# Kernel tuning notes

Measured on AMD Instinct MI355X. Metric: run time of the kernel, lower is better.

## Reference

```python
import jax, jax.numpy as jnp
import numpy as np

HIDDEN = 2048
HEADS = 16
HEAD_DIM = HIDDEN // HEADS          # 128
HALF = HEAD_DIM // 2                # 64
LATENT = HIDDEN // 4                # 512 (compression_ratio=4)
ROPE_BASE = 10000.0


def _rope_cos_sin(seq_len):
    # LlamaRotaryEmbedding with dim=HALF
    inv_freq = 1.0 / (ROPE_BASE ** (jnp.arange(0, HALF, 2, dtype=jnp.float32) / HALF))
    t = jnp.arange(seq_len, dtype=jnp.float32)
    freqs = jnp.einsum('i,j->ij', t, inv_freq)          # [S, HALF/2]
    emb = jnp.concatenate([freqs, freqs], axis=-1)       # [S, HALF]
    cos = jnp.cos(emb)[None, :, None, :]                 # [1,S,1,HALF]
    sin = jnp.sin(emb)[None, :, None, :]
    return cos, sin


def _rotate_half(x):
    x1, x2 = jnp.split(x, 2, axis=-1)
    return jnp.concatenate([-x2, x1], axis=-1)


def _apply_rope(x, cos, sin):
    return x * cos + _rotate_half(x) * sin


def setup_inputs() -> dict:
    key = jax.random.key(0)
    ks = jax.random.split(key, 10)
    B, S = 2, 2048
    std = 0.02
    inp = {
        'x':        jax.random.normal(ks[0], (B, S, HIDDEN), jnp.float32),
        # weights stored as [in, out] (transposed torch Linear weight)
        'W_kv_d':   jax.random.normal(ks[1], (HIDDEN, LATENT), jnp.float32) * std,
        'W_q_d':    jax.random.normal(ks[2], (HIDDEN, LATENT), jnp.float32) * std,
        'W_k_u':    jax.random.normal(ks[3], (LATENT, HEADS * HALF), jnp.float32) * std,
        'W_q_u':    jax.random.normal(ks[4], (LATENT, HEADS * HALF), jnp.float32) * std,
        'W_v_u':    jax.random.normal(ks[5], (LATENT, HIDDEN), jnp.float32) * std,
        'W_rope_k': jax.random.normal(ks[6], (HIDDEN, HIDDEN // 2), jnp.float32) * std,
        'W_rope_q': jax.random.normal(ks[7], (LATENT, HIDDEN // 2), jnp.float32) * std,
        'W_o':      jax.random.normal(ks[8], (HIDDEN, HIDDEN), jnp.float32) * std,
    }
    return inp


def reference(x, W_kv_d, W_q_d, W_k_u, W_q_u, W_v_u, W_rope_k, W_rope_q, W_o):
    B, S, _ = x.shape
    kv_latent = x @ W_kv_d                      # [B,S,LATENT]
    q_latent = x @ W_q_d                        # [B,S,LATENT]

    k = (kv_latent @ W_k_u).reshape(B, S, HEADS, HALF)
    q = (q_latent @ W_q_u).reshape(B, S, HEADS, HALF)
    v = (kv_latent @ W_v_u).reshape(B, S, HEADS, HEAD_DIM)

    q_rope = (q_latent @ W_rope_q).reshape(B, S, HEADS, HALF)
    k_rope = (x @ W_rope_k).reshape(B, S, HEADS, HALF)

    cos, sin = _rope_cos_sin(S)
    k_rope = _apply_rope(k_rope, cos, sin)
    q_rope = _apply_rope(q_rope, cos, sin)

    q = jnp.concatenate([q, q_rope], axis=-1)   # [B,S,H,HEAD_DIM]
    k = jnp.concatenate([k, k_rope], axis=-1)

    scale = 1.0 / jnp.sqrt(jnp.float32(HEAD_DIM))
    scores = jnp.einsum('bqhd,bkhd->bhqk', q, k) * scale   # [B,H,S,S]
    causal = jnp.tril(jnp.ones((S, S), dtype=bool))
    scores = jnp.where(causal[None, None], scores, jnp.float32(-1e30))
    attn = jax.nn.softmax(scores, axis=-1)
    y = jnp.einsum('bhqk,bkhd->bqhd', attn, v).reshape(B, S, HIDDEN)
    return y @ W_o
```

## Files before the change

kernel.cpp:

```cpp
#include <hip/hip_runtime.h>
#include <hip/hip_bf16.h>

typedef __hip_bfloat16 bf16;
typedef __attribute__((ext_vector_type(8))) short short8;
typedef __attribute__((ext_vector_type(4))) float f32x4;

#define AS1 __attribute__((address_space(1)))
#define AS3 __attribute__((address_space(3)))

__device__ __forceinline__ void gload_lds16(const bf16* gp, bf16* lp) {
  __builtin_amdgcn_global_load_lds((const AS1 void*)gp, (AS3 void*)lp, 16, 0, 0);
}

__device__ __forceinline__ float fast_exp2(float x) {
#if __has_builtin(__builtin_amdgcn_exp2f)
  return __builtin_amdgcn_exp2f(x);
#else
  return exp2f(x);
#endif
}

__device__ __forceinline__ void store_c(bf16* C, size_t idx, float v) { C[idx] = __float2bfloat16(v); }
__device__ __forceinline__ void store_c(float* C, size_t idx, float v) { C[idx] = v; }

struct __align__(8) b16x4 { bf16 a, b, c, d; };

__global__ void cvt_f32_bf16(const float* __restrict__ in, bf16* __restrict__ out) {
  const int i = (blockIdx.x * 256 + threadIdx.x) * 4;
  const float4 v = *(const float4*)(in + i);
  out[i + 0] = __float2bfloat16(v.x);
  out[i + 1] = __float2bfloat16(v.y);
  out[i + 2] = __float2bfloat16(v.z);
  out[i + 3] = __float2bfloat16(v.w);
}

__global__ void rope_tab_kernel(float2* __restrict__ ctab) {
  const int idx = blockIdx.x * 256 + threadIdx.x;
  const int i = idx & 31;
  const int s = idx >> 5;
  const float inv = fast_exp2(-(float)i * 0.41524101186092029f);
  const float ang = (float)s * inv;
  ctab[idx] = make_float2(cosf(ang), sinf(ang));
}

struct PrepArgs {
  const float* src[8];
  bf16* dst[8];
  int R[8], C[8], cum[8];
};

__global__ void prep_kernel(PrepArgs a) {
  __shared__ bf16 t[32][33];
  const int blk = blockIdx.x;
  int e = 0;
  while (e < 7 && blk >= a.cum[e]) ++e;
  const int lt = blk - (e ? a.cum[e - 1] : 0);
  const int R = a.R[e], C = a.C[e];
  const int tpr = C >> 5;
  const int bx = lt % tpr, by = lt / tpr;
  const float* in = a.src[e];
  bf16* out = a.dst[e];
  const int c0 = bx * 32, r0 = by * 32;
  const int tx = threadIdx.x, ty = threadIdx.y;
  for (int i = 0; i < 4; ++i)
    t[ty + 8 * i][tx] = __float2bfloat16(in[(size_t)(r0 + ty + 8 * i) * C + c0 + tx]);
  __syncthreads();
  for (int i = 0; i < 4; ++i)
    out[(size_t)(c0 + ty + 8 * i) * R + r0 + tx] = t[tx][ty + 8 * i];
}

template <typename CT, int MODE>
__global__ void gemm_bt(const bf16* __restrict__ A, int lda,
                        const bf16* __restrict__ Bt,
                        CT* __restrict__ C, bf16* __restrict__ C2, int ldc,
                        int K, const float2* __restrict__ ctab)
{
  __shared__ __align__(16) bf16 As[2][128 * 32];
  __shared__ __align__(16) bf16 Bs[2][128 * 32];
  const int tid  = threadIdx.x;
  const int wave = tid >> 6, lane = tid & 63;
  const int quad = lane >> 4, l16 = lane & 15;
  const int m0 = blockIdx.y * 128, n0 = blockIdx.x * 128;
  const int wm = (wave >> 1) * 64, wn = (wave & 1) * 64;

  f32x4 acc[4][4];
#pragma unroll
  for (int i = 0; i < 4; ++i)
#pragma unroll
    for (int j = 0; j < 4; ++j) acc[i][j] = (f32x4){0.f, 0.f, 0.f, 0.f};

  const int r1  = tid >> 2;
  const int ks1 = (tid & 3) * 8;

  gload_lds16(A  + (size_t)(m0 + r1)      * lda + ks1, &As[0][tid * 8]);
  gload_lds16(A  + (size_t)(m0 + r1 + 64) * lda + ks1, &As[0][(tid + 256) * 8]);
  gload_lds16(Bt + (size_t)(n0 + r1)      * K   + ks1, &Bs[0][tid * 8]);
  gload_lds16(Bt + (size_t)(n0 + r1 + 64) * K   + ks1, &Bs[0][(tid + 256) * 8]);

  int cur = 0;
  for (int k0 = 0; k0 < K; k0 += 32) {
    if (k0 + 32 < K) {
      const int kn = k0 + 32;
      const int nxt = cur ^ 1;
      gload_lds16(A  + (size_t)(m0 + r1)      * lda + kn + ks1, &As[nxt][tid * 8]);
      gload_lds16(A  + (size_t)(m0 + r1 + 64) * lda + kn + ks1, &As[nxt][(tid + 256) * 8]);
      gload_lds16(Bt + (size_t)(n0 + r1)      * K   + kn + ks1, &Bs[nxt][tid * 8]);
      gload_lds16(Bt + (size_t)(n0 + r1 + 64) * K   + kn + ks1, &Bs[nxt][(tid + 256) * 8]);
      asm volatile("s_waitcnt vmcnt(4)" ::: "memory");
    } else {
      asm volatile("s_waitcnt vmcnt(0)" ::: "memory");
    }
    __builtin_amdgcn_s_barrier();

    short8 af[4], bf_[4];
#pragma unroll
    for (int mt = 0; mt < 4; ++mt)
      af[mt] = *(const short8*)&As[cur][(wm + mt * 16 + l16) * 32 + quad * 8];
#pragma unroll
    for (int nt = 0; nt < 4; ++nt)
      bf_[nt] = *(const short8*)&Bs[cur][(wn + nt * 16 + l16) * 32 + quad * 8];
#pragma unroll
    for (int mt = 0; mt < 4; ++mt)
#pragma unroll
      for (int nt = 0; nt < 4; ++nt)
        acc[mt][nt] = __builtin_amdgcn_mfma_f32_16x16x32_bf16(af[mt], bf_[nt], acc[mt][nt], 0, 0, 0);
    __builtin_amdgcn_s_barrier();
    cur ^= 1;
  }

  if (MODE == 0) {
#pragma unroll
    for (int mt = 0; mt < 4; ++mt) {
      const int row = m0 + wm + mt * 16 + quad * 4;
#pragma unroll
      for (int nt = 0; nt < 4; ++nt) {
        const int cn = n0 + wn + nt * 16 + l16;
        const f32x4 v = acc[mt][nt];
#pragma unroll
        for (int r = 0; r < 4; ++r)
          store_c(C, (size_t)(row + r) * ldc + cn, v[r]);
      }
    }
  } else if (MODE == 4) {
    if (n0 < 1024) {
#pragma unroll
      for (int mt = 0; mt < 4; ++mt) {
        const int row = m0 + wm + mt * 16 + quad * 4;
#pragma unroll
        for (int nt = 0; nt < 4; ++nt) {
          const int cn = n0 + wn + nt * 16 + l16;
          const f32x4 v = acc[mt][nt];
#pragma unroll
          for (int r = 0; r < 4; ++r)
            store_c(C, (size_t)(row + r) * 1024 + cn, v[r]);
        }
      }
    } else {
#pragma unroll
      for (int mt = 0; mt < 4; ++mt) {
        const int row = m0 + wm + mt * 16 + quad * 4;
        f32x4 w[4];
#pragma unroll
        for (int nt = 0; nt < 4; ++nt) w[nt] = acc[mt][nt];
#pragma unroll
        for (int r = 0; r < 4; ++r) {
          const int s = (row + r) & 2047;
          const float2 cs0 = ctab[(s << 5) + l16];
          const float2 cs1 = ctab[(s << 5) + 16 + l16];
          const float x1a = w[0][r], x2a = w[2][r];
          const float x1b = w[1][r], x2b = w[3][r];
          w[0][r] = x1a * cs0.x - x2a * cs0.y;
          w[2][r] = x2a * cs0.x + x1a * cs0.y;
          w[1][r] = x1b * cs1.x - x2b * cs1.y;
          w[3][r] = x2b * cs1.x + x1b * cs1.y;
        }
#pragma unroll
        for (int nt = 0; nt < 4; ++nt) {
          const int cn2 = n0 + wn + nt * 16 + l16 - 1024;
          const int g = ((cn2 >> 6) << 7) + 64 + (cn2 & 63);
#pragma unroll
          for (int r = 0; r < 4; ++r)
            C2[(size_t)(row + r) * 2048 + g] = __float2bfloat16(w[nt][r]);
        }
      }
    }
  }
}

__global__ void gemm_up_fused(const bf16* __restrict__ latcat,
                              const bf16* __restrict__ wtUP,
                              const bf16* __restrict__ wtQcat,
                              bf16* __restrict__ vT, bf16* __restrict__ kfull,
                              bf16* __restrict__ qfull,
                              const float2* __restrict__ ctab)
{
  const bool is2 = (blockIdx.x >= 24);
  const bf16* A  = latcat + (is2 ? 512 : 0);
  const bf16* Bt = is2 ? wtQcat : wtUP;
  const int n0 = (is2 ? (int)blockIdx.x - 24 : (int)blockIdx.x) * 128;
  const int K = 512, lda = 1024;

  __shared__ __align__(16) bf16 As[2][128 * 32];
  __shared__ __align__(16) bf16 Bs[2][128 * 32];
  const int tid  = threadIdx.x;
  const int wave = tid >> 6, lane = tid & 63;
  const int quad = lane >> 4, l16 = lane & 15;
  const int m0 = blockIdx.y * 128;
  const int wm = (wave >> 1) * 64, wn = (wave & 1) * 64;

  f32x4 acc[4][4];
#pragma unroll
  for (int i = 0; i < 4; ++i)
#pragma unroll
    for (int j = 0; j < 4; ++j) acc[i][j] = (f32x4){0.f, 0.f, 0.f, 0.f};

  const int r1  = tid >> 2;
  const int ks1 = (tid & 3) * 8;

  gload_lds16(A  + (size_t)(m0 + r1)      * lda + ks1, &As[0][tid * 8]);
  gload_lds16(A  + (size_t)(m0 + r1 + 64) * lda + ks1, &As[0][(tid + 256) * 8]);
  gload_lds16(Bt + (size_t)(n0 + r1)      * K   + ks1, &Bs[0][tid * 8]);
  gload_lds16(Bt + (size_t)(n0 + r1 + 64) * K   + ks1, &Bs[0][(tid + 256) * 8]);

  int cur = 0;
  for (int k0 = 0; k0 < K; k0 += 32) {
    if (k0 + 32 < K) {
      const int kn = k0 + 32;
      const int nxt = cur ^ 1;
      gload_lds16(A  + (size_t)(m0 + r1)      * lda + kn + ks1, &As[nxt][tid * 8]);
      gload_lds16(A  + (size_t)(m0 + r1 + 64) * lda + kn + ks1, &As[nxt][(tid + 256) * 8]);
      gload_lds16(Bt + (size_t)(n0 + r1)      * K   + kn + ks1, &Bs[nxt][tid * 8]);
      gload_lds16(Bt + (size_t)(n0 + r1 + 64) * K   + kn + ks1, &Bs[nxt][(tid + 256) * 8]);
      asm volatile("s_waitcnt vmcnt(4)" ::: "memory");
    } else {
      asm volatile("s_waitcnt vmcnt(0)" ::: "memory");
    }
    __builtin_amdgcn_s_barrier();

    short8 af[4], bf_[4];
#pragma unroll
    for (int mt = 0; mt < 4; ++mt)
      af[mt] = *(const short8*)&As[cur][(wm + mt * 16 + l16) * 32 + quad * 8];
#pragma unroll
    for (int nt = 0; nt < 4; ++nt)
      bf_[nt] = *(const short8*)&Bs[cur][(wn + nt * 16 + l16) * 32 + quad * 8];
#pragma unroll
    for (int mt = 0; mt < 4; ++mt)
#pragma unroll
      for (int nt = 0; nt < 4; ++nt)
        acc[mt][nt] = __builtin_amdgcn_mfma_f32_16x16x32_bf16(af[mt], bf_[nt], acc[mt][nt], 0, 0, 0);
    __builtin_amdgcn_s_barrier();
    cur ^= 1;
  }

  if (is2) {
    if (n0 < 1024) {
#pragma unroll
      for (int mt = 0; mt < 4; ++mt) {
        const int row = m0 + wm + mt * 16 + quad * 4;
#pragma unroll
        for (int nt = 0; nt < 4; ++nt) {
          const int cn = n0 + wn + nt * 16 + l16;
          const int g = (((cn >> 6) & 15) << 7) + ((cn >> 10) << 6) + (cn & 63);
          const f32x4 v = acc[mt][nt];
#pragma unroll
          for (int r = 0; r < 4; ++r)
            qfull[(size_t)(row + r) * 2048 + g] = __float2bfloat16(v[r]);
        }
      }
    } else {
#pragma unroll
      for (int mt = 0; mt < 4; ++mt) {
        const int row = m0 + wm + mt * 16 + quad * 4;
        f32x4 w[4];
#pragma unroll
        for (int nt = 0; nt < 4; ++nt) w[nt] = acc[mt][nt];
#pragma unroll
        for (int r = 0; r < 4; ++r) {
          const int s = (row + r) & 2047;
          const float2 cs0 = ctab[(s << 5) + l16];
          const float2 cs1 = ctab[(s << 5) + 16 + l16];
          const float x1a = w[0][r], x2a = w[2][r];
          const float x1b = w[1][r], x2b = w[3][r];
          w[0][r] = x1a * cs0.x - x2a * cs0.y;
          w[2][r] = x2a * cs0.x + x1a * cs0.y;
          w[1][r] = x1b * cs1.x - x2b * cs1.y;
          w[3][r] = x2b * cs1.x + x1b * cs1.y;
        }
#pragma unroll
        for (int nt = 0; nt < 4; ++nt) {
          const int cn = n0 + wn + nt * 16 + l16;
          const int g = (((cn >> 6) & 15) << 7) + ((cn >> 10) << 6) + (cn & 63);
#pragma unroll
          for (int r = 0; r < 4; ++r)
            qfull[(size_t)(row + r) * 2048 + g] = __float2bfloat16(w[nt][r]);
        }
      }
    }
  } else {
#pragma unroll
    for (int mt = 0; mt < 4; ++mt) {
      const int row = m0 + wm + mt * 16 + quad * 4;
#pragma unroll
      for (int nt = 0; nt < 4; ++nt) {
        const int cn = n0 + wn + nt * 16 + l16;
        const f32x4 v = acc[mt][nt];
        if (cn < 1024) {
          const int g = ((cn >> 6) << 7) + (cn & 63);
#pragma unroll
          for (int r = 0; r < 4; ++r)
            kfull[(size_t)(row + r) * 2048 + g] = __float2bfloat16(v[r]);
        } else {
          const int cn2 = cn - 1024;
          const int bb = row >> 11, s0 = row & 2047;
          b16x4 pk;
          pk.a = __float2bfloat16(v[0]); pk.b = __float2bfloat16(v[1]);
          pk.c = __float2bfloat16(v[2]); pk.d = __float2bfloat16(v[3]);
          *(b16x4*)(vT + ((size_t)(bb * 2048 + cn2)) * 2048 + s0) = pk;
        }
      }
    }
  }
}

__device__ __forceinline__ void attn_phase(
    const bf16* __restrict__ Q, const bf16* __restrict__ Kf,
    const bf16* __restrict__ VT,
    size_t kqbase, size_t vtbase, int qt, int t0, int t1,
    bf16* __restrict__ Ks, bf16* __restrict__ VTs, bf16* __restrict__ Psw,
    f32x4 (&o)[2][8], f32x4 (&lacc)[2], const short8 ones,
    int wave, int quad, int l16, int krow, int kcol, int vrow, int vcol)
{
  const float C2 = 0.08838834764831845f * 1.4426950408889634f;
  const float MNEG = -30.0f;
  const int wq0 = qt * 128 + wave * 32;

  short8 qf[2][4];
#pragma unroll
  for (int m = 0; m < 2; ++m) {
    const bf16* qp = Q + kqbase + (size_t)(wq0 + m * 16 + l16) * 2048 + quad * 8;
#pragma unroll
    for (int kc = 0; kc < 4; ++kc) qf[m][kc] = *(const short8*)(qp + kc * 32);
  }

  short8 kg[4], vg[4];
  {
    const int kk = t0 * 64;
#pragma unroll
    for (int i = 0; i < 4; ++i)
      kg[i] = *(const short8*)(Kf + kqbase + (size_t)(kk + krow + i * 16) * 2048 + kcol);
#pragma unroll
    for (int i = 0; i < 4; ++i)
      vg[i] = *(const short8*)(VT + vtbase + (size_t)(vrow + i * 32) * 2048 + kk + vcol);
  }

  for (int t = t0; t < t1; ++t) {
    const int k0 = t * 64;
    __syncthreads();
#pragma unroll
    for (int i = 0; i < 4; ++i) {
      const int rw = krow + i * 16;
      *(short8*)&Ks[rw * 128 + (kcol ^ ((rw & 7) * 8))] = kg[i];
    }
#pragma unroll
    for (int i = 0; i < 4; ++i) {
      const int rw = vrow + i * 32;
      *(short8*)&VTs[rw * 64 + (vcol ^ ((rw & 7) * 8))] = vg[i];
    }
    __syncthreads();
    if (t + 1 < t1) {
      const int kn = k0 + 64;
#pragma unroll
      for (int i = 0; i < 4; ++i)
        kg[i] = *(const short8*)(Kf + kqbase + (size_t)(kn + krow + i * 16) * 2048 + kcol);
#pragma unroll
      for (int i = 0; i < 4; ++i)
        vg[i] = *(const short8*)(VT + vtbase + (size_t)(vrow + i * 32) * 2048 + kn + vcol);
    }
    if (k0 > wq0 + 31) continue;

    f32x4 sf[2][4];
#pragma unroll
    for (int kt = 0; kt < 4; ++kt) {
      sf[0][kt] = (f32x4){0, 0, 0, 0};
      sf[1][kt] = (f32x4){0, 0, 0, 0};
    }
#pragma unroll
    for (int kt = 0; kt < 4; ++kt) {
#pragma unroll
      for (int kc = 0; kc < 4; ++kc) {
        const short8 bfr = *(const short8*)&Ks[(kt * 16 + l16) * 128 +
                                              ((kc * 32 + quad * 8) ^ ((l16 & 7) * 8))];
        sf[0][kt] = __builtin_amdgcn_mfma_f32_16x16x32_bf16(qf[0][kc], bfr, sf[0][kt], 0, 0, 0);
        sf[1][kt] = __builtin_amdgcn_mfma_f32_16x16x32_bf16(qf[1][kc], bfr, sf[1][kt], 0, 0, 0);
      }
    }
#pragma unroll
    for (int m = 0; m < 2; ++m) {
      const int row0m = wq0 + m * 16 + quad * 4;
      if (k0 + 63 > row0m) {
#pragma unroll
        for (int kt = 0; kt < 4; ++kt) {
          const int col = k0 + kt * 16 + l16;
#pragma unroll
          for (int r = 0; r < 4; ++r)
            sf[m][kt][r] = (col > row0m + r) ? -3e38f : sf[m][kt][r];
        }
      }
    }
#pragma unroll
    for (int m = 0; m < 2; ++m)
#pragma unroll
      for (int kt = 0; kt < 4; ++kt)
#pragma unroll
        for (int r = 0; r < 4; ++r) {
          const float p = fast_exp2(__builtin_fmaf(sf[m][kt][r], C2, MNEG));
          const int prow = m * 16 + quad * 4 + r;
          const int pcol = (kt * 16 + l16) ^ (quad * 16);
          Psw[prow * 64 + pcol] = __float2bfloat16(p);
        }
    asm volatile("s_waitcnt lgkmcnt(0)" ::: "memory");
#pragma unroll
    for (int kc = 0; kc < 2; ++kc) {
      short8 ap[2];
      const int acol = (kc * 32 + quad * 8) ^ (((l16 >> 2) & 3) * 16);
      ap[0] = *(const short8*)&Psw[l16 * 64 + acol];
      lacc[0] = __builtin_amdgcn_mfma_f32_16x16x32_bf16(ap[0], ones, lacc[0], 0, 0, 0);
      ap[1] = *(const short8*)&Psw[(16 + l16) * 64 + acol];
      lacc[1] = __builtin_amdgcn_mfma_f32_16x16x32_bf16(ap[1], ones, lacc[1], 0, 0, 0);
#pragma unroll
      for (int dt = 0; dt < 8; ++dt) {
        const short8 vb = *(const short8*)&VTs[(dt * 16 + l16) * 64 +
                                              ((kc * 32 + quad * 8) ^ ((l16 & 7) * 8))];
        o[0][dt] = __builtin_amdgcn_mfma_f32_16x16x32_bf16(ap[0], vb, o[0][dt], 0, 0, 0);
        o[1][dt] = __builtin_amdgcn_mfma_f32_16x16x32_bf16(ap[1], vb, o[1][dt], 0, 0, 0);
      }
    }
  }
}

__global__ __launch_bounds__(256, 2) void attn10_kernel(
    const bf16* __restrict__ Q, const bf16* __restrict__ Kf,
    const bf16* __restrict__ VT, bf16* __restrict__ Y,
    bf16* __restrict__ poA, float* __restrict__ lA, float* __restrict__ lB)
{
  __shared__ __align__(16) bf16 Ks[64 * 128];
  __shared__ __align__(16) bf16 VTs[128 * 64];
  __shared__ __align__(16) bf16 Ps[4 * 32 * 64];
  const int tid  = threadIdx.x;
  const int wave = tid >> 6, lane = tid & 63;
  const int quad = lane >> 4, l16 = lane & 15;
  const int bh = blockIdx.x;
  const int j  = blockIdx.y;
  const int qt_A = 15 - j;
  const int qt_B = j;
  const size_t kqbase = ((size_t)(bh >> 4) * 2048) * 2048 + (bh & 15) * 128;
  const size_t vtbase = (size_t)bh * 128 * 2048;

  short8 ones;
#pragma unroll
  for (int i = 0; i < 8; ++i) ones[i] = (short)0x3F80;

  const int krow = tid >> 4, kcol = (tid & 15) * 8;
  const int vrow = tid >> 3, vcol = (tid & 7) * 8;
  bf16* Psw = Ps + wave * (32 * 64);

  f32x4 o[2][8];
  f32x4 lacc[2];

#pragma unroll
  for (int m = 0; m < 2; ++m)
#pragma unroll
    for (int i = 0; i < 8; ++i) o[m][i] = (f32x4){0, 0, 0, 0};
  lacc[0] = (f32x4){0, 0, 0, 0};
  lacc[1] = (f32x4){0, 0, 0, 0};
  attn_phase(Q, Kf, VT, kqbase, vtbase, qt_A, qt_A + 1, 2 * qt_A + 2,
             Ks, VTs, Psw, o, lacc, ones, wave, quad, l16, krow, kcol, vrow, vcol);
  {
    bf16* po = poA + ((size_t)(bh * 16 + qt_A) << 14);
    float* pl = lA + ((bh * 16 + qt_A) << 7);
#pragma unroll
    for (int m = 0; m < 2; ++m)
#pragma unroll
      for (int r = 0; r < 4; ++r) {
        const int rl = wave * 32 + m * 16 + quad * 4 + r;
#pragma unroll
        for (int dt = 0; dt < 8; ++dt)
          po[rl * 128 + dt * 16 + l16] = __float2bfloat16(o[m][dt][r]);
        if (l16 == 0) pl[rl] = lacc[m][r];
      }
  }

#pragma unroll
  for (int m = 0; m < 2; ++m)
#pragma unroll
    for (int i = 0; i < 8; ++i) o[m][i] = (f32x4){0, 0, 0, 0};
  lacc[0] = (f32x4){0, 0, 0, 0};
  lacc[1] = (f32x4){0, 0, 0, 0};
  attn_phase(Q, Kf, VT, kqbase, vtbase, qt_B, 0, qt_B + 1,
             Ks, VTs, Psw, o, lacc, ones, wave, quad, l16, krow, kcol, vrow, vcol);
  {
    float* pl = lB + ((bh * 16 + qt_B) << 7);
#pragma unroll
    for (int m = 0; m < 2; ++m)
#pragma unroll
      for (int r = 0; r < 4; ++r) {
        const int rl = wave * 32 + m * 16 + quad * 4 + r;
#pragma unroll
        for (int dt = 0; dt < 8; ++dt)
          Y[kqbase + (size_t)(qt_B * 128 + rl) * 2048 + dt * 16 + l16] =
              __float2bfloat16(o[m][dt][r]);
        if (l16 == 0) pl[rl] = lacc[m][r];
      }
  }
}

__global__ void attn_merge(bf16* __restrict__ Y, const bf16* __restrict__ poA,
                           const float* __restrict__ lA, const float* __restrict__ lB)
{
  const int t = blockIdx.x * 256 + threadIdx.x;
  const size_t e = (size_t)t * 8;
  const int col = (int)(e & 2047);
  const int row = (int)(e >> 11);
  const int b = row >> 11, s = row & 2047;
  const int h = col >> 7, dcol = col & 127;
  const int bh = b * 16 + h, qt = s >> 7, rl = s & 127;
  const int li = ((bh * 16 + qt) << 7) + rl;
  const float inv = 1.0f / (lA[li] + lB[li]);
  const short8 va = *(const short8*)(poA + (((size_t)(bh * 16 + qt)) << 14) + rl * 128 + dcol);
  const short8 vb = *(const short8*)(Y + e);
  short8 out;
#pragma unroll
  for (int i = 0; i < 8; ++i) {
    const float fa = __bfloat162float(((const bf16*)&va)[i]);
    const float fb = __bfloat162float(((const bf16*)&vb)[i]);
    ((bf16*)&out)[i] = __float2bfloat16((fa + fb) * inv);
  }
  *(short8*)(Y + e) = out;
}

extern "C" void kernel_launch(void* const* d_in, const int* in_sizes, int n_in,
                              void* d_out, int out_size, void* d_ws, size_t ws_size,
                              hipStream_t stream)
{
  const float* x      = (const float*)d_in[0];
  const float* Wkvd   = (const float*)d_in[1];
  const float* Wqd    = (const float*)d_in[2];
  const float* Wku    = (const float*)d_in[3];
  const float* Wqu    = (const float*)d_in[4];
  const float* Wvu    = (const float*)d_in[5];
  const float* Wropek = (const float*)d_in[6];
  const float* Wropeq = (const float*)d_in[7];
  const float* Wo     = (const float*)d_in[8];

  char* ws = (char*)d_ws;
  size_t off = 0;
  auto alloc = [&](size_t elems) {
    bf16* p = (bf16*)(ws + off);
    off += ((elems * sizeof(bf16) + 255) & ~(size_t)255);
    return p;
  };
  bf16* wtX    = alloc((size_t)2048 * 2048);
  bf16* wtUP   = alloc((size_t)3072 * 512);
  bf16* wtQcat = alloc((size_t)2048 * 512);
  bf16* latcat = alloc((size_t)4096 * 1024);
  bf16* wt_o   = alloc((size_t)2048 * 2048);
  bf16* xbf    = alloc((size_t)4096 * 2048);
  bf16* qfull  = alloc((size_t)4096 * 2048);
  bf16* kfull  = alloc((size_t)4096 * 2048);
  float2* ctab = (float2*)alloc((size_t)65536 * 4);
  bf16* ybuf   = (bf16*)ws;
  bf16* vT     = (bf16*)d_out;
  bf16*  poA = xbf;
  float* lA  = (float*)(ws + 16777216);
  float* lB  = (float*)(ws + 16777216 + 262144);
  (void)ws_size; (void)in_sizes; (void)n_in; (void)out_size;

  rope_tab_kernel<<<256, 256, 0, stream>>>(ctab);
  cvt_f32_bf16<<<8192, 256, 0, stream>>>(x, xbf);

  PrepArgs pa;
  const float* srcs[8] = {Wkvd, Wqd, Wropek, Wku, Wvu, Wqu, Wropeq, Wo};
  bf16* dsts[8] = {wtX, wtX + (size_t)512 * 2048, wtX + (size_t)1024 * 2048,
                   wtUP, wtUP + (size_t)1024 * 512,
                   wtQcat, wtQcat + (size_t)1024 * 512, wt_o};
  const int Rs[8] = {2048, 2048, 2048, 512, 512, 512, 512, 2048};
  const int Cs[8] = {512, 512, 1024, 1024, 2048, 1024, 1024, 2048};
  int cum = 0;
  for (int e = 0; e < 8; ++e) {
    pa.src[e] = srcs[e]; pa.dst[e] = dsts[e]; pa.R[e] = Rs[e]; pa.C[e] = Cs[e];
    cum += (Rs[e] >> 5) * (Cs[e] >> 5);
    pa.cum[e] = cum;
  }
  prep_kernel<<<cum, dim3(32, 8), 0, stream>>>(pa);

  gemm_bt<bf16, 4><<<dim3(16, 32), 256, 0, stream>>>(xbf, 2048, wtX, latcat, kfull, 1024, 2048, ctab);
  gemm_up_fused<<<dim3(40, 32), 256, 0, stream>>>(latcat, wtUP, wtQcat, vT, kfull, qfull, ctab);

  attn10_kernel<<<dim3(32, 16), 256, 0, stream>>>(qfull, kfull, vT, ybuf, poA, lA, lB);
  attn_merge<<<4096, 256, 0, stream>>>(ybuf, poA, lA, lB);
  gemm_bt<float, 0><<<dim3(16, 32), 256, 0, stream>>>(ybuf, 2048, wt_o, (float*)d_out, (bf16*)nullptr, 2048, 2048, ctab);
}
```

Measured before the change: 325.0 us.

## Merge preprocessing kernels and split-K the output projection with atomic accumulation

The f32-to-bf16 conversion of x, the RoPE table build and the weight transpose/convert kernels are folded into one launch that picks its role from the block index. This saves two kernel launches and lets the work overlap within one grid. The final W_o GEMM is split along K into two halves via a z grid dimension, and each half adds into a zeroed fp32 output with atomicAdd. This doubles the block count to fill more CUs, at the cost of a 32MB memset and atomic write traffic.

```diff
diff --git a/kernel.cpp b/kernel.cpp
--- a/kernel.cpp
+++ b/kernel.cpp
@@ -25,43 +25,47 @@
 
 struct __align__(8) b16x4 { bf16 a, b, c, d; };
 
-__global__ void cvt_f32_bf16(const float* __restrict__ in, bf16* __restrict__ out) {
-  const int i = (blockIdx.x * 256 + threadIdx.x) * 4;
-  const float4 v = *(const float4*)(in + i);
-  out[i + 0] = __float2bfloat16(v.x);
-  out[i + 1] = __float2bfloat16(v.y);
-  out[i + 2] = __float2bfloat16(v.z);
-  out[i + 3] = __float2bfloat16(v.w);
-}
-
-__global__ void rope_tab_kernel(float2* __restrict__ ctab) {
-  const int idx = blockIdx.x * 256 + threadIdx.x;
-  const int i = idx & 31;
-  const int s = idx >> 5;
-  const float inv = fast_exp2(-(float)i * 0.41524101186092029f);
-  const float ang = (float)s * inv;
-  ctab[idx] = make_float2(cosf(ang), sinf(ang));
-}
-
 struct PrepArgs {
   const float* src[8];
   bf16* dst[8];
   int R[8], C[8], cum[8];
 };
 
-__global__ void prep_kernel(PrepArgs a) {
+__global__ void prep_all(const float* __restrict__ x, bf16* __restrict__ xbf,
+                         float2* __restrict__ ctab, PrepArgs a)
+{
+  const int blk = blockIdx.x;
+  const int tid = threadIdx.x;
+  if (blk < 8192) {
+    const int i = (blk * 256 + tid) * 4;
+    const float4 v = *(const float4*)(x + i);
+    xbf[i + 0] = __float2bfloat16(v.x);
+    xbf[i + 1] = __float2bfloat16(v.y);
+    xbf[i + 2] = __float2bfloat16(v.z);
+    xbf[i + 3] = __float2bfloat16(v.w);
+    return;
+  }
+  if (blk < 8448) {
+    const int idx = (blk - 8192) * 256 + tid;
+    const int i = idx & 31;
+    const int s = idx >> 5;
+    const float inv = fast_exp2(-(float)i * 0.41524101186092029f);
+    const float ang = (float)s * inv;
+    ctab[idx] = make_float2(cosf(ang), sinf(ang));
+    return;
+  }
   __shared__ bf16 t[32][33];
-  const int blk = blockIdx.x;
+  const int pb = blk - 8448;
   int e = 0;
-  while (e < 7 && blk >= a.cum[e]) ++e;
-  const int lt = blk - (e ? a.cum[e - 1] : 0);
+  while (e < 7 && pb >= a.cum[e]) ++e;
+  const int lt = pb - (e ? a.cum[e - 1] : 0);
   const int R = a.R[e], C = a.C[e];
   const int tpr = C >> 5;
   const int bx = lt % tpr, by = lt / tpr;
   const float* in = a.src[e];
   bf16* out = a.dst[e];
   const int c0 = bx * 32, r0 = by * 32;
-  const int tx = threadIdx.x, ty = threadIdx.y;
+  const int tx = tid & 31, ty = tid >> 5;
   for (int i = 0; i < 4; ++i)
     t[ty + 8 * i][tx] = __float2bfloat16(in[(size_t)(r0 + ty + 8 * i) * C + c0 + tx]);
   __syncthreads();
@@ -83,6 +87,10 @@
   const int m0 = blockIdx.y * 128, n0 = blockIdx.x * 128;
   const int wm = (wave >> 1) * 64, wn = (wave & 1) * 64;
 
+  const int kspan = (MODE == 0) ? (K >> 1) : K;
+  const int kbase = (MODE == 0) ? (int)blockIdx.z * kspan : 0;
+  const int kend  = kbase + kspan;
+
   f32x4 acc[4][4];
 #pragma unroll
   for (int i = 0; i < 4; ++i)
@@ -92,14 +100,14 @@
   const int r1  = tid >> 2;
   const int ks1 = (tid & 3) * 8;
 
-  gload_lds16(A  + (size_t)(m0 + r1)      * lda + ks1, &As[0][tid * 8]);
-  gload_lds16(A  + (size_t)(m0 + r1 + 64) * lda + ks1, &As[0][(tid + 256) * 8]);
-  gload_lds16(Bt + (size_t)(n0 + r1)      * K   + ks1, &Bs[0][tid * 8]);
-  gload_lds16(Bt + (size_t)(n0 + r1 + 64) * K   + ks1, &Bs[0][(tid + 256) * 8]);
+  gload_lds16(A  + (size_t)(m0 + r1)      * lda + kbase + ks1, &As[0][tid * 8]);
+  gload_lds16(A  + (size_t)(m0 + r1 + 64) * lda + kbase + ks1, &As[0][(tid + 256) * 8]);
+  gload_lds16(Bt + (size_t)(n0 + r1)      * K   + kbase + ks1, &Bs[0][tid * 8]);
+  gload_lds16(Bt + (size_t)(n0 + r1 + 64) * K   + kbase + ks1, &Bs[0][(tid + 256) * 8]);
 
   int cur = 0;
-  for (int k0 = 0; k0 < K; k0 += 32) {
-    if (k0 + 32 < K) {
+  for (int k0 = kbase; k0 < kend; k0 += 32) {
+    if (k0 + 32 < kend) {
       const int kn = k0 + 32;
       const int nxt = cur ^ 1;
       gload_lds16(A  + (size_t)(m0 + r1)      * lda + kn + ks1, &As[nxt][tid * 8]);
@@ -138,7 +146,7 @@
         const f32x4 v = acc[mt][nt];
 #pragma unroll
         for (int r = 0; r < 4; ++r)
-          store_c(C, (size_t)(row + r) * ldc + cn, v[r]);
+          atomicAdd((float*)&C[(size_t)(row + r) * ldc + cn], v[r]);
       }
     }
   } else if (MODE == 4) {
@@ -576,9 +584,6 @@
   float* lB  = (float*)(ws + 16777216 + 262144);
   (void)ws_size; (void)in_sizes; (void)n_in; (void)out_size;
 
-  rope_tab_kernel<<<256, 256, 0, stream>>>(ctab);
-  cvt_f32_bf16<<<8192, 256, 0, stream>>>(x, xbf);
-
   PrepArgs pa;
   const float* srcs[8] = {Wkvd, Wqd, Wropek, Wku, Wvu, Wqu, Wropeq, Wo};
   bf16* dsts[8] = {wtX, wtX + (size_t)512 * 2048, wtX + (size_t)1024 * 2048,
@@ -592,12 +597,14 @@
     cum += (Rs[e] >> 5) * (Cs[e] >> 5);
     pa.cum[e] = cum;
   }
-  prep_kernel<<<cum, dim3(32, 8), 0, stream>>>(pa);
+  prep_all<<<8448 + cum, 256, 0, stream>>>(x, xbf, ctab, pa);
 
   gemm_bt<bf16, 4><<<dim3(16, 32), 256, 0, stream>>>(xbf, 2048, wtX, latcat, kfull, 1024, 2048, ctab);
   gemm_up_fused<<<dim3(40, 32), 256, 0, stream>>>(latcat, wtUP, wtQcat, vT, kfull, qfull, ctab);
 
   attn10_kernel<<<dim3(32, 16), 256, 0, stream>>>(qfull, kfull, vT, ybuf, poA, lA, lB);
   attn_merge<<<4096, 256, 0, stream>>>(ybuf, poA, lA, lB);
-  gemm_bt<float, 0><<<dim3(16, 32), 256, 0, stream>>>(ybuf, 2048, wt_o, (float*)d_out, (bf16*)nullptr, 2048, 2048, ctab);
-}
+
+  hipMemsetAsync(d_out, 0, (size_t)4096 * 2048 * sizeof(float), stream);
+  gemm_bt<float, 0><<<dim3(16, 32, 2), 256, 0, stream>>>(ybuf, 2048, wt_o, (float*)d_out, (bf16*)nullptr, 2048, 2048, ctab);
+}
```

Result: slower. 362.2 us (+11.4%).
